# Optimization experiments

Measured on AMD Instinct MI355X. Metric: run time of the kernel, lower is better.

Reference implementation:

```python
import jax, jax.numpy as jnp
import numpy as np

N, E, L = 10000, 160000, 4
IN, HID, HEADS, OUT = 15, 128, 4, 5
C = HID              # per-head out_channels of TransformerConv
HC = HEADS * C       # concatenated width = 512
EPS = 1e-5


def _w(k, shape, fan_in):
    return (jax.random.normal(k, shape, jnp.float32) / np.sqrt(fan_in)).astype(jnp.float32)


def setup_inputs() -> dict:
    key = jax.random.key(0)
    ks = jax.random.split(key, 24)
    return {
        "x": jax.random.normal(ks[0], (N, IN), jnp.float32),
        "edge_index": jax.random.randint(ks[1], (2, E), 0, N, dtype=jnp.int32),
        # input / output projections
        "W_in": _w(ks[2], (IN, HID), IN), "b_in": jnp.zeros((HID,), jnp.float32),
        "W_out": _w(ks[3], (HID, OUT), HID), "b_out": jnp.zeros((OUT,), jnp.float32),
        # stacked per-layer TransformerConv params (L leading dim)
        "Wq": _w(ks[4], (L, HID, HC), HID), "bq": jnp.zeros((L, HC), jnp.float32),
        "Wk": _w(ks[5], (L, HID, HC), HID), "bk": jnp.zeros((L, HC), jnp.float32),
        "Wv": _w(ks[6], (L, HID, HC), HID), "bv": jnp.zeros((L, HC), jnp.float32),
        "Wskip": _w(ks[7], (L, HID, HC), HID), "bskip": jnp.zeros((L, HC), jnp.float32),
        "Wbeta": _w(ks[8], (L, 3 * HC, 1), 3 * HC),
        "ln_w": jnp.ones((L, HC), jnp.float32), "ln_b": jnp.zeros((L, HC), jnp.float32),
        "Wproj": _w(ks[9], (L, HC, HID), HC), "bproj": jnp.zeros((L, HID), jnp.float32),
    }


def _forward(x, edge_index, W_in, b_in, Wq, bq, Wk, bk, Wv, bv,
             Wskip, bskip, Wbeta, ln_w, ln_b, Wproj, bproj, W_out, b_out):
    src, dst = edge_index[0], edge_index[1]  # message j->i aggregated at dst
    h = x @ W_in + b_in  # [N, HID]

    def layer(h, p):
        Wq_, bq_, Wk_, bk_, Wv_, bv_, Ws_, bs_, Wb_, lw, lb, Wp_, bp_ = p
        q = (h @ Wq_ + bq_).reshape(N, HEADS, C)
        k = (h @ Wk_ + bk_).reshape(N, HEADS, C)
        v = (h @ Wv_ + bv_).reshape(N, HEADS, C)
        # attention logits per edge/head: [E, HEADS]
        logits = (q[dst] * k[src]).sum(-1) / jnp.sqrt(jnp.float32(C))
        # segment softmax over incoming edges of each target node
        m = jax.ops.segment_max(logits, dst, num_segments=N)
        ex = jnp.exp(logits - m[dst])
        den = jax.ops.segment_sum(ex, dst, num_segments=N)
        alpha = ex / (den[dst] + 1e-16)
        out = jax.ops.segment_sum(v[src] * alpha[..., None], dst,
                                  num_segments=N).reshape(N, HC)
        # beta-gated skip (TransformerConv beta=True)
        skip = h @ Ws_ + bs_
        beta = jax.nn.sigmoid(jnp.concatenate([out, skip, out - skip], -1) @ Wb_)  # [N,1]
        out = beta * skip + (1.0 - beta) * out
        # PyG LayerNorm, mode='graph' (single graph): normalize over all elements
        xc = out - out.mean()
        out = xc / (jnp.sqrt((xc * xc).mean()) + EPS) * lw + lb
        out = out @ Wp_ + bp_
        return jax.nn.relu(out + h), None

    params = (Wq, bq, Wk, bk, Wv, bv, Wskip, bskip, Wbeta, ln_w, ln_b, Wproj, bproj)
    h, _ = jax.lax.scan(layer, h, params)
    return h @ W_out + b_out


def reference(x, edge_index, W_in, b_in, Wq, bq, Wk, bk, Wv, bv,
              Wskip, bskip, Wbeta, ln_w, ln_b, Wproj, bproj, W_out, b_out):
    return _forward(x, edge_index, W_in, b_in, Wq, bq, Wk, bk, Wv, bv,
                    Wskip, bskip, Wbeta, ln_w, ln_b, Wproj, bproj, W_out, b_out)
```

## Files before the change

kernel.cpp:

```cpp
#include <hip/hip_runtime.h>
#include <math.h>

#define NN 10000
#define NE 160000
#define HCW 512
#define CH 128
#define NLAYERS 4
#define LN_EPS 1e-5f
#define NBUCK 128

typedef short bf16x8 __attribute__((ext_vector_type(8)));
typedef float f32x4 __attribute__((ext_vector_type(4)));

__device__ inline unsigned short f2bf(float f) {
    union { float f; unsigned int u; } x; x.f = f;
    unsigned int u = x.u;
    return (unsigned short)((u + 0x7FFFu + ((u >> 16) & 1u)) >> 16);
}
__device__ inline float bf2f(unsigned short s) {
    union { unsigned int u; float f; } x; x.u = ((unsigned int)s) << 16;
    return x.f;
}
__device__ inline float lo16(unsigned int u) {
    union { unsigned int x; float f; } v; v.x = u << 16; return v.f;
}
__device__ inline float hi16(unsigned int u) {
    union { unsigned int x; float f; } v; v.x = u & 0xffff0000u; return v.f;
}

template<int CTRL>
__device__ inline float dppadd(float x) {
    int y = __builtin_amdgcn_update_dpp(0, __float_as_int(x), CTRL, 0xF, 0xF, true);
    return x + __int_as_float(y);
}
__device__ inline float red16(float x) {
    x = dppadd<0x128>(x);
    x = dppadd<0x124>(x);
    x = dppadd<0x122>(x);
    x = dppadd<0x121>(x);
    return x;
}
__device__ inline float red64(float x) {
    x = red16(x);
    x += __shfl_xor(x, 16, 64);
    x += __shfl_xor(x, 32, 64);
    return x;
}

__device__ inline float dot8(const float4& q0, const float4& q1, const uint4& kk) {
    return q0.x * lo16(kk.x) + q0.y * hi16(kk.x)
         + q0.z * lo16(kk.y) + q0.w * hi16(kk.y)
         + q1.x * lo16(kk.z) + q1.y * hi16(kk.z)
         + q1.z * lo16(kk.w) + q1.w * hi16(kk.w);
}

__global__ void k_init(int* cnt, int* fill, float* stats) {
    int i = blockIdx.x * blockDim.x + threadIdx.x;
    if (i < NN) { cnt[i] = 0; fill[i] = 0; }
    if (i < NLAYERS * NBUCK * 16) stats[i] = 0.f;
}

__global__ void k_count(const int* __restrict__ dst, int* __restrict__ cnt) {
    int e = blockIdx.x * blockDim.x + threadIdx.x;
    if (e < NE) atomicAdd(&cnt[dst[e]], 1);
}

__global__ __launch_bounds__(1024) void k_scan(const int* __restrict__ cnt, int* __restrict__ offs) {
    __shared__ int sh[1024];
    __shared__ int carry;
    if (threadIdx.x == 0) carry = 0;
    __syncthreads();
    for (int base = 0; base < NN; base += 1024) {
        int i = base + threadIdx.x;
        int v = (i < NN) ? cnt[i] : 0;
        sh[threadIdx.x] = v;
        __syncthreads();
        for (int off = 1; off < 1024; off <<= 1) {
            int t = (threadIdx.x >= off) ? sh[threadIdx.x - off] : 0;
            __syncthreads();
            sh[threadIdx.x] += t;
            __syncthreads();
        }
        int incl = sh[threadIdx.x];
        if (i < NN) offs[i] = carry + incl - v;
        __syncthreads();
        if (threadIdx.x == 1023) carry += sh[1023];
        __syncthreads();
    }
    if (threadIdx.x == 0) offs[NN] = carry;
}

__global__ void k_fill(const int* __restrict__ src, const int* __restrict__ dst,
                       const int* __restrict__ offs, int* __restrict__ fill,
                       int* __restrict__ col) {
    int e = blockIdx.x * blockDim.x + threadIdx.x;
    if (e < NE) {
        int d = dst[e];
        int p = offs[d] + atomicAdd(&fill[d], 1);
        col[p] = src[e];
    }
}

__global__ void k_wconv(const float* __restrict__ Wq, const float* __restrict__ Wk,
                        const float* __restrict__ Wv, const float* __restrict__ Ws,
                        const float* __restrict__ Wp,
                        unsigned short* __restrict__ wt_qkvs,
                        unsigned short* __restrict__ wpt) {
    int id = blockIdx.x * blockDim.x + threadIdx.x;
    if (id < NLAYERS * 2048 * 128) {
        int l = id >> 18;
        int rem = id & 262143;
        int n = rem >> 7, k = rem & 127;
        int mat = n >> 9, wcol = n & 511;
        const float* W = (mat == 0) ? Wq : (mat == 1) ? Wk : (mat == 2) ? Wv : Ws;
        wt_qkvs[id] = f2bf(W[(size_t)l * 65536 + k * 512 + wcol]);
    } else if (id < NLAYERS * 2048 * 128 + NLAYERS * 128 * 512) {
        int id2 = id - NLAYERS * 2048 * 128;
        int l = id2 >> 16;
        int rem = id2 & 65535;
        int n = rem >> 9, k = rem & 511;
        wpt[(size_t)l * 65536 + n * 512 + k] = f2bf(Wp[(size_t)l * 65536 + k * 128 + n]);
    }
}

__global__ __launch_bounds__(128) void k_inproj(const float* __restrict__ x,
                                                const float* __restrict__ W,
                                                const float* __restrict__ b,
                                                float* __restrict__ h,
                                                unsigned short* __restrict__ h_bf) {
    int n = blockIdx.x;
    int j = threadIdx.x;
    float acc = b[j];
#pragma unroll
    for (int i = 0; i < 15; i++) acc += x[n * 15 + i] * W[i * 128 + j];
    h[n * 128 + j] = acc;
    h_bf[n * 128 + j] = f2bf(acc);
}

__global__ __launch_bounds__(256) void k_qkvs_mfma(
    const unsigned short* __restrict__ h_bf,
    const unsigned short* __restrict__ Wt,
    const float* __restrict__ bq, const float* __restrict__ bk,
    const float* __restrict__ bv, const float* __restrict__ bs,
    unsigned short* __restrict__ qb16, unsigned short* __restrict__ kv16,
    unsigned short* __restrict__ sb16) {
    __shared__ unsigned short As[128 * 128];
    __shared__ unsigned short Bs[128 * 128];
    int row0 = blockIdx.x * 128;
    int n0 = blockIdx.y * 128;
    int t = threadIdx.x;
#pragma unroll
    for (int i = 0; i < 8; i++) {
        int c = t + i * 256;
        int r = c >> 4, cc = c & 15;
        int gr = row0 + r;
        uint4 v = make_uint4(0, 0, 0, 0);
        if (gr < NN) v = *(const uint4*)(h_bf + (size_t)gr * 128 + cc * 8);
        int sc = (r << 4) | (cc ^ (r & 7));
        *(uint4*)(As + sc * 8) = v;
    }
#pragma unroll
    for (int i = 0; i < 8; i++) {
        int c = t + i * 256;
        int r = c >> 4, cc = c & 15;
        uint4 v = *(const uint4*)(Wt + (size_t)(n0 + r) * 128 + cc * 8);
        int sc = (r << 4) | (cc ^ (r & 7));
        *(uint4*)(Bs + sc * 8) = v;
    }
    __syncthreads();
    int wave = t >> 6, lane = t & 63;
    int wr = (wave >> 1) * 64, wc = (wave & 1) * 64;
    int lr = lane & 15, lk = lane >> 4;
    f32x4 acc[4][4] = {};
#pragma unroll
    for (int ks = 0; ks < 4; ks++) {
        bf16x8 a[4], b[4];
#pragma unroll
        for (int mi = 0; mi < 4; mi++) {
            int r = wr + mi * 16 + lr;
            int cc = (ks * 4 + lk) ^ (r & 7);
            a[mi] = *(const bf16x8*)(As + (((r << 4) | cc) * 8));
        }
#pragma unroll
        for (int ni = 0; ni < 4; ni++) {
            int r = wc + ni * 16 + lr;
            int cc = (ks * 4 + lk) ^ (r & 7);
            b[ni] = *(const bf16x8*)(Bs + (((r << 4) | cc) * 8));
        }
#pragma unroll
        for (int mi = 0; mi < 4; mi++)
#pragma unroll
            for (int ni = 0; ni < 4; ni++)
                acc[mi][ni] = __builtin_amdgcn_mfma_f32_16x16x32_bf16(a[mi], b[ni], acc[mi][ni], 0, 0, 0);
    }
    int mat = blockIdx.y >> 2;
    int wcol0 = n0 & 511;
    const float* bias_p = (mat == 0) ? bq : (mat == 1) ? bk : (mat == 2) ? bv : bs;
    __syncthreads();
#pragma unroll
    for (int ni = 0; ni < 4; ni++) {
        int colL = wc + ni * 16 + lr;
        float bias = bias_p[wcol0 + colL];
#pragma unroll
        for (int mi = 0; mi < 4; mi++) {
            int rowB = wr + mi * 16 + 4 * lk;
#pragma unroll
            for (int r = 0; r < 4; r++) {
                int row = rowB + r;
                unsigned int w = (unsigned int)(row * 64 + (colL >> 1));
                w ^= ((row >> 2) & 7) << 3;
                As[w * 2 + (colL & 1)] = f2bf(acc[mi][ni][r] + bias);
            }
        }
    }
    __syncthreads();
    unsigned short* outp = (mat == 0) ? qb16 : (mat == 3) ? sb16 : kv16;
    int rowStride = (mat == 1 || mat == 2) ? 1024 : 512;
    int cbase = wcol0 + ((mat == 2) ? 512 : 0);
#pragma unroll
    for (int i = 0; i < 8; i++) {
        int idx = t + i * 256;
        int row2 = idx >> 4;
        int c8 = (idx & 15) * 8;
        int gr = row0 + row2;
        if (gr < NN) {
            unsigned int wb = (unsigned int)(row2 * 64 + (idx & 15) * 4);
            wb ^= ((row2 >> 2) & 7) << 3;
            uint4 v = *(const uint4*)(As + wb * 2);
            *(uint4*)(outp + (size_t)gr * rowStride + cbase + c8) = v;
        }
    }
}

__global__ __launch_bounds__(256) void k_attn_beta(
    const unsigned short* __restrict__ qb16,
    const unsigned short* __restrict__ kv16,
    const unsigned short* __restrict__ sb16,
    const float* __restrict__ Wb,
    const int* __restrict__ offs, const int* __restrict__ col,
    unsigned short* __restrict__ gated16, float* __restrict__ stats) {
    int n = blockIdx.x;
    int head = threadIdx.x >> 6;
    int lane = threadIdx.x & 63;
    int g = lane >> 4;
    int subl = lane & 15;
    const int hbase = head * CH;
    const int off = hbase + subl * 8;
    uint4 qq = *(const uint4*)(qb16 + (size_t)n * HCW + off);
    float4 q0 = {lo16(qq.x), hi16(qq.x), lo16(qq.y), hi16(qq.y)};
    float4 q1 = {lo16(qq.z), hi16(qq.z), lo16(qq.w), hi16(qq.w)};
    int beg = offs[n], end = offs[n + 1];
    const float scale = 0.08838834764831845f;

    float mA = -INFINITY, sA = 0.f, mB = -INFINITY, sB = 0.f;
    float4 a0A = {0.f, 0.f, 0.f, 0.f}, a1A = {0.f, 0.f, 0.f, 0.f};
    float4 a0B = {0.f, 0.f, 0.f, 0.f}, a1B = {0.f, 0.f, 0.f, 0.f};

    for (int p = beg + g; p < end; p += 8) {
        int pB = p + 4;
        bool hasB = (pB < end);
        int snA = col[p];
        int snB = hasB ? col[pB] : snA;
        const unsigned short* bA = kv16 + ((size_t)snA << 10) + off;
        const unsigned short* bB = kv16 + ((size_t)snB << 10) + off;
        uint4 kkA = *(const uint4*)bA;
        uint4 vvA = *(const uint4*)(bA + 512);
        uint4 kkB = *(const uint4*)bB;
        uint4 vvB = *(const uint4*)(bB + 512);
        float dA = dot8(q0, q1, kkA);
        float dB = dot8(q0, q1, kkB);
        dA = red16(dA);
        dB = red16(dB);
        float lA = dA * scale;
        float lB = dB * scale;
        if (lA <= mA + 8.f) {
            float w = __expf(lA - mA);
            sA += w;
            a0A.x += w * lo16(vvA.x); a0A.y += w * hi16(vvA.x);
            a0A.z += w * lo16(vvA.y); a0A.w += w * hi16(vvA.y);
            a1A.x += w * lo16(vvA.z); a1A.y += w * hi16(vvA.z);
            a1A.z += w * lo16(vvA.w); a1A.w += w * hi16(vvA.w);
        } else {
            float sc = __expf(mA - lA);
            sA = sA * sc + 1.f;
            a0A.x = a0A.x * sc + lo16(vvA.x); a0A.y = a0A.y * sc + hi16(vvA.x);
            a0A.z = a0A.z * sc + lo16(vvA.y); a0A.w = a0A.w * sc + hi16(vvA.y);
            a1A.x = a1A.x * sc + lo16(vvA.z); a1A.y = a1A.y * sc + hi16(vvA.z);
            a1A.z = a1A.z * sc + lo16(vvA.w); a1A.w = a1A.w * sc + hi16(vvA.w);
            mA = lA;
        }
        if (hasB) {
            if (lB <= mB + 8.f) {
                float w = __expf(lB - mB);
                sB += w;
                a0B.x += w * lo16(vvB.x); a0B.y += w * hi16(vvB.x);
                a0B.z += w * lo16(vvB.y); a0B.w += w * hi16(vvB.y);
                a1B.x += w * lo16(vvB.z); a1B.y += w * hi16(vvB.z);
                a1B.z += w * lo16(vvB.w); a1B.w += w * hi16(vvB.w);
            } else {
                float sc = __expf(mB - lB);
                sB = sB * sc + 1.f;
                a0B.x = a0B.x * sc + lo16(vvB.x); a0B.y = a0B.y * sc + hi16(vvB.x);
                a0B.z = a0B.z * sc + lo16(vvB.y); a0B.w = a0B.w * sc + hi16(vvB.y);
                a1B.x = a1B.x * sc + lo16(vvB.z); a1B.y = a1B.y * sc + hi16(vvB.z);
                a1B.z = a1B.z * sc + lo16(vvB.w); a1B.w = a1B.w * sc + hi16(vvB.w);
                mB = lB;
            }
        }
    }
    {
        float mn = fmaxf(mA, mB);
        float c1 = (sA > 0.f) ? __expf(mA - mn) : 0.f;
        float c2 = (sB > 0.f) ? __expf(mB - mn) : 0.f;
        sA = sA * c1 + sB * c2;
        a0A.x = a0A.x * c1 + a0B.x * c2; a0A.y = a0A.y * c1 + a0B.y * c2;
        a0A.z = a0A.z * c1 + a0B.z * c2; a0A.w = a0A.w * c1 + a0B.w * c2;
        a1A.x = a1A.x * c1 + a1B.x * c2; a1A.y = a1A.y * c1 + a1B.y * c2;
        a1A.z = a1A.z * c1 + a1B.z * c2; a1A.w = a1A.w * c1 + a1B.w * c2;
        mA = mn;
    }
#pragma unroll
    for (int off2 = 16; off2 <= 32; off2 <<= 1) {
        float m_o = __shfl_xor(mA, off2, 64);
        float s_o = __shfl_xor(sA, off2, 64);
        float4 b0, b1;
        b0.x = __shfl_xor(a0A.x, off2, 64); b0.y = __shfl_xor(a0A.y, off2, 64);
        b0.z = __shfl_xor(a0A.z, off2, 64); b0.w = __shfl_xor(a0A.w, off2, 64);
        b1.x = __shfl_xor(a1A.x, off2, 64); b1.y = __shfl_xor(a1A.y, off2, 64);
        b1.z = __shfl_xor(a1A.z, off2, 64); b1.w = __shfl_xor(a1A.w, off2, 64);
        float mn = fmaxf(mA, m_o);
        float c1 = (sA > 0.f) ? __expf(mA - mn) : 0.f;
        float c2 = (s_o > 0.f) ? __expf(m_o - mn) : 0.f;
        sA = sA * c1 + s_o * c2;
        a0A.x = a0A.x * c1 + b0.x * c2; a0A.y = a0A.y * c1 + b0.y * c2;
        a0A.z = a0A.z * c1 + b0.z * c2; a0A.w = a0A.w * c1 + b0.w * c2;
        a1A.x = a1A.x * c1 + b1.x * c2; a1A.y = a1A.y * c1 + b1.y * c2;
        a1A.z = a1A.z * c1 + b1.z * c2; a1A.w = a1A.w * c1 + b1.w * c2;
        mA = mn;
    }
    float inv = (sA > 0.f) ? 1.f / sA : 0.f;

    __shared__ float att_s[512];
    if (g == 0) {
        float4 o0 = {a0A.x * inv, a0A.y * inv, a0A.z * inv, a0A.w * inv};
        float4 o1 = {a1A.x * inv, a1A.y * inv, a1A.z * inv, a1A.w * inv};
        *(float4*)(att_s + off) = o0;
        *(float4*)(att_s + off + 4) = o1;
    }
    __syncthreads();

    int c0 = hbase + lane * 2;
    float o0 = att_s[c0], o1 = att_s[c0 + 1];
    unsigned int sku = *(const unsigned int*)(sb16 + (size_t)n * HCW + c0);
    float skx = lo16(sku), sky = hi16(sku);
    float part = o0 * Wb[c0] + o1 * Wb[c0 + 1]
               + skx * Wb[512 + c0] + sky * Wb[512 + c0 + 1]
               + (o0 - skx) * Wb[1024 + c0] + (o1 - sky) * Wb[1024 + c0 + 1];
    part = red64(part);
    __shared__ float red[4];
    if (lane == 0) red[head] = part;
    __syncthreads();
    float tot = red[0] + red[1] + red[2] + red[3];
    float beta = 1.f / (1.f + __expf(-tot));
    float gx = beta * skx + (1.f - beta) * o0;
    float gy = beta * sky + (1.f - beta) * o1;
    unsigned int gu = (unsigned int)f2bf(gx) | ((unsigned int)f2bf(gy) << 16);
    *(unsigned int*)(gated16 + (size_t)n * HCW + c0) = gu;

    float gxr = lo16(gu), gyr = hi16(gu);
    float ls = red64(gxr + gyr);
    float lq = red64(gxr * gxr + gyr * gyr);
    __shared__ float r2[8];
    if (lane == 0) { r2[head] = ls; r2[4 + head] = lq; }
    __syncthreads();
    if (threadIdx.x == 0) {
        int b = n & (NBUCK - 1);
        atomicAdd(&stats[b * 16], r2[0] + r2[1] + r2[2] + r2[3]);
        atomicAdd(&stats[b * 16 + 1], r2[4] + r2[5] + r2[6] + r2[7]);
    }
}

__global__ __launch_bounds__(512) void k_proj_mfma(
    const unsigned short* __restrict__ gated16,
    const unsigned short* __restrict__ Wpt,
    const float* __restrict__ bp,
    const float* __restrict__ lw, const float* __restrict__ lb,
    const float* __restrict__ stats,
    float* __restrict__ h, unsigned short* __restrict__ h_bf) {
    __shared__ unsigned short As[64 * 128];
    __shared__ unsigned short Bs[128 * 128];
    int row0 = blockIdx.x * 64;
    int t = threadIdx.x;
    float ssum = 0.f, sq = 0.f;
#pragma unroll 16
    for (int i = 0; i < NBUCK; i++) { ssum += stats[i * 16]; sq += stats[i * 16 + 1]; }
    const float invM = 1.f / (NN * 512.f);
    float mean = ssum * invM;
    float ms = sq * invM - mean * mean;
    float rstd = 1.f / (sqrtf(fmaxf(ms, 0.f)) + LN_EPS);
    int wave = t >> 6, lane = t & 63;
    int wr = (wave >> 1) * 16, wc = (wave & 1) * 64;
    int lr = lane & 15, lk = lane >> 4;
    f32x4 acc[4] = {};
    for (int kc = 0; kc < 4; kc++) {
        __syncthreads();
#pragma unroll
        for (int i = 0; i < 2; i++) {
            int c = t + i * 512;
            int r = c >> 4, cc = c & 15;
            int gr = row0 + r;
            int gk = kc * 128 + cc * 8;
            unsigned short u[8];
            if (gr < NN) {
                uint4 gv = *(const uint4*)(gated16 + (size_t)gr * 512 + gk);
                float vals[8] = {lo16(gv.x), hi16(gv.x), lo16(gv.y), hi16(gv.y),
                                 lo16(gv.z), hi16(gv.z), lo16(gv.w), hi16(gv.w)};
#pragma unroll
                for (int j = 0; j < 8; j++)
                    u[j] = f2bf((vals[j] - mean) * rstd * lw[gk + j] + lb[gk + j]);
            } else {
#pragma unroll
                for (int j = 0; j < 8; j++) u[j] = 0;
            }
            int sc = (r << 4) | (cc ^ (r & 7));
            *(uint4*)(As + sc * 8) = *(uint4*)u;
        }
#pragma unroll
        for (int i = 0; i < 4; i++) {
            int c = t + i * 512;
            int r = c >> 4, cc = c & 15;
            uint4 v = *(const uint4*)(Wpt + (size_t)r * 512 + kc * 128 + cc * 8);
            int sc = (r << 4) | (cc ^ (r & 7));
            *(uint4*)(Bs + sc * 8) = v;
        }
        __syncthreads();
#pragma unroll
        for (int ks = 0; ks < 4; ks++) {
            bf16x8 a, b[4];
            {
                int r = wr + lr;
                int cc = (ks * 4 + lk) ^ (r & 7);
                a = *(const bf16x8*)(As + (((r << 4) | cc) * 8));
            }
#pragma unroll
            for (int ni = 0; ni < 4; ni++) {
                int r = wc + ni * 16 + lr;
                int cc = (ks * 4 + lk) ^ (r & 7);
                b[ni] = *(const bf16x8*)(Bs + (((r << 4) | cc) * 8));
            }
#pragma unroll
            for (int ni = 0; ni < 4; ni++)
                acc[ni] = __builtin_amdgcn_mfma_f32_16x16x32_bf16(a, b[ni], acc[ni], 0, 0, 0);
        }
    }
#pragma unroll
    for (int ni = 0; ni < 4; ni++) {
        int gc = wc + ni * 16 + lr;
        float bias = bp[gc];
        int gr0 = row0 + wr + 4 * lk;
#pragma unroll
        for (int r = 0; r < 4; r++) {
            int grr = gr0 + r;
            if (grr < NN) {
                float o = acc[ni][r] + bias + h[(size_t)grr * 128 + gc];
                o = fmaxf(o, 0.f);
                h[(size_t)grr * 128 + gc] = o;
                h_bf[(size_t)grr * 128 + gc] = f2bf(o);
            }
        }
    }
}

__global__ void k_out(const float* __restrict__ h, const float* __restrict__ W,
                      const float* __restrict__ b, float* __restrict__ out) {
    int i = blockIdx.x * blockDim.x + threadIdx.x;
    if (i >= NN * 5) return;
    int n = i / 5, j = i % 5;
    float acc = b[j];
    for (int k = 0; k < 128; k++) acc += h[(size_t)n * 128 + k] * W[k * 5 + j];
    out[i] = acc;
}

extern "C" void kernel_launch(void* const* d_in, const int* in_sizes, int n_in,
                              void* d_out, int out_size, void* d_ws, size_t ws_size,
                              hipStream_t stream) {
    const float* x     = (const float*)d_in[0];
    const int* ei      = (const int*)d_in[1];
    const float* W_in  = (const float*)d_in[2];
    const float* b_in  = (const float*)d_in[3];
    const float* W_out = (const float*)d_in[4];
    const float* b_out = (const float*)d_in[5];
    const float* Wq    = (const float*)d_in[6];
    const float* bq    = (const float*)d_in[7];
    const float* Wk    = (const float*)d_in[8];
    const float* bk    = (const float*)d_in[9];
    const float* Wv    = (const float*)d_in[10];
    const float* bv    = (const float*)d_in[11];
    const float* Wsk   = (const float*)d_in[12];
    const float* bsk   = (const float*)d_in[13];
    const float* Wbeta = (const float*)d_in[14];
    const float* ln_w  = (const float*)d_in[15];
    const float* ln_b  = (const float*)d_in[16];
    const float* Wproj = (const float*)d_in[17];
    const float* bproj = (const float*)d_in[18];
    float* out = (float*)d_out;

    float* h     = (float*)d_ws;
    float* stats = h + (size_t)NN * 128;
    int* offs = (int*)(stats + NLAYERS * NBUCK * 16);
    int* cnt  = offs + (NN + 1);
    int* fill = cnt + NN;
    int* col  = fill + NN;
    unsigned short* h_bf = (unsigned short*)(((uintptr_t)(col + NE) + 15) & ~(uintptr_t)15);
    unsigned short* qb16 = h_bf + (size_t)NN * 128;
    unsigned short* sb16 = qb16 + (size_t)NN * 512;
    unsigned short* kv16 = sb16 + (size_t)NN * 512;
    unsigned short* wt_qkvs = kv16 + (size_t)NN * 1024;
    unsigned short* wpt = wt_qkvs + (size_t)NLAYERS * 2048 * 128;
    unsigned short* gated16 = qb16;

    const int* src = ei;
    const int* dst = ei + NE;

    k_init<<<(NN + 255) / 256, 256, 0, stream>>>(cnt, fill, stats);
    k_count<<<(NE + 255) / 256, 256, 0, stream>>>(dst, cnt);
    k_scan<<<1, 1024, 0, stream>>>(cnt, offs);
    k_fill<<<(NE + 255) / 256, 256, 0, stream>>>(src, dst, offs, fill, col);
    {
        int tot = NLAYERS * 2048 * 128 + NLAYERS * 128 * 512;
        k_wconv<<<(tot + 255) / 256, 256, 0, stream>>>(Wq, Wk, Wv, Wsk, Wproj, wt_qkvs, wpt);
    }
    k_inproj<<<NN, 128, 0, stream>>>(x, W_in, b_in, h, h_bf);

    for (int l = 0; l < NLAYERS; ++l) {
        const unsigned short* Wt_ = wt_qkvs + (size_t)l * 2048 * 128;
        const unsigned short* Wp_ = wpt + (size_t)l * 128 * 512;
        const float* bq_ = bq + l * 512;
        const float* bk_ = bk + l * 512;
        const float* bv_ = bv + l * 512;
        const float* bs_ = bsk + l * 512;
        const float* Wb_ = Wbeta + (size_t)l * 1536;
        const float* lw_ = ln_w + l * 512;
        const float* lb_ = ln_b + l * 512;
        const float* bp_ = bproj + l * 128;
        float* st = stats + (size_t)l * NBUCK * 16;

        dim3 g1((NN + 127) / 128, 16);
        k_qkvs_mfma<<<g1, 256, 0, stream>>>(h_bf, Wt_, bq_, bk_, bv_, bs_,
                                            qb16, kv16, sb16);
        k_attn_beta<<<NN, 256, 0, stream>>>(qb16, kv16, sb16, Wb_, offs, col, gated16, st);
        k_proj_mfma<<<(NN + 63) / 64, 512, 0, stream>>>(gated16, Wp_, bp_, lw_, lb_, st, h, h_bf);
    }
    k_out<<<(NN * 5 + 255) / 256, 256, 0, stream>>>(h, W_out, b_out, out);
}
```

Measured before the change: 453.0 us.

## Map one wavefront per node in attention kernel with 4-edge unrolled gathers

The attention/beta kernel now assigns one 64-lane wavefront per destination node (4 nodes per block) instead of a whole 256-thread block per node. Each lane covers 8 channels across all heads, and the edge loop gathers 4 neighbors at once into independent online-softmax accumulators. This removes the cross-wave LDS exchange, two __syncthreads, and the cross-group shuffle merge, and raises memory-level parallelism per lane. The trade-off is more registers per thread, and each edge's gather now goes through a single wave serially rather than across 4 edge groups, so per-node latency for high-degree nodes grows.

```diff
diff --git a/kernel.cpp b/kernel.cpp
--- a/kernel.cpp
+++ b/kernel.cpp
@@ -239,142 +239,108 @@
     const float* __restrict__ Wb,
     const int* __restrict__ offs, const int* __restrict__ col,
     unsigned short* __restrict__ gated16, float* __restrict__ stats) {
-    int n = blockIdx.x;
-    int head = threadIdx.x >> 6;
+    int wave = threadIdx.x >> 6;
     int lane = threadIdx.x & 63;
-    int g = lane >> 4;
-    int subl = lane & 15;
-    const int hbase = head * CH;
-    const int off = hbase + subl * 8;
+    int n = blockIdx.x * 4 + wave;
+    const int off = ((lane >> 4) << 7) + ((lane & 15) << 3);
     uint4 qq = *(const uint4*)(qb16 + (size_t)n * HCW + off);
     float4 q0 = {lo16(qq.x), hi16(qq.x), lo16(qq.y), hi16(qq.y)};
     float4 q1 = {lo16(qq.z), hi16(qq.z), lo16(qq.w), hi16(qq.w)};
     int beg = offs[n], end = offs[n + 1];
     const float scale = 0.08838834764831845f;
 
-    float mA = -INFINITY, sA = 0.f, mB = -INFINITY, sB = 0.f;
-    float4 a0A = {0.f, 0.f, 0.f, 0.f}, a1A = {0.f, 0.f, 0.f, 0.f};
-    float4 a0B = {0.f, 0.f, 0.f, 0.f}, a1B = {0.f, 0.f, 0.f, 0.f};
-
-    for (int p = beg + g; p < end; p += 8) {
-        int pB = p + 4;
-        bool hasB = (pB < end);
-        int snA = col[p];
-        int snB = hasB ? col[pB] : snA;
-        const unsigned short* bA = kv16 + ((size_t)snA << 10) + off;
-        const unsigned short* bB = kv16 + ((size_t)snB << 10) + off;
-        uint4 kkA = *(const uint4*)bA;
-        uint4 vvA = *(const uint4*)(bA + 512);
-        uint4 kkB = *(const uint4*)bB;
-        uint4 vvB = *(const uint4*)(bB + 512);
-        float dA = dot8(q0, q1, kkA);
-        float dB = dot8(q0, q1, kkB);
-        dA = red16(dA);
-        dB = red16(dB);
-        float lA = dA * scale;
-        float lB = dB * scale;
-        if (lA <= mA + 8.f) {
-            float w = __expf(lA - mA);
-            sA += w;
-            a0A.x += w * lo16(vvA.x); a0A.y += w * hi16(vvA.x);
-            a0A.z += w * lo16(vvA.y); a0A.w += w * hi16(vvA.y);
-            a1A.x += w * lo16(vvA.z); a1A.y += w * hi16(vvA.z);
-            a1A.z += w * lo16(vvA.w); a1A.w += w * hi16(vvA.w);
-        } else {
-            float sc = __expf(mA - lA);
-            sA = sA * sc + 1.f;
-            a0A.x = a0A.x * sc + lo16(vvA.x); a0A.y = a0A.y * sc + hi16(vvA.x);
-            a0A.z = a0A.z * sc + lo16(vvA.y); a0A.w = a0A.w * sc + hi16(vvA.y);
-            a1A.x = a1A.x * sc + lo16(vvA.z); a1A.y = a1A.y * sc + hi16(vvA.z);
-            a1A.z = a1A.z * sc + lo16(vvA.w); a1A.w = a1A.w * sc + hi16(vvA.w);
-            mA = lA;
-        }
-        if (hasB) {
-            if (lB <= mB + 8.f) {
-                float w = __expf(lB - mB);
-                sB += w;
-                a0B.x += w * lo16(vvB.x); a0B.y += w * hi16(vvB.x);
-                a0B.z += w * lo16(vvB.y); a0B.w += w * hi16(vvB.y);
-                a1B.x += w * lo16(vvB.z); a1B.y += w * hi16(vvB.z);
-                a1B.z += w * lo16(vvB.w); a1B.w += w * hi16(vvB.w);
+    float m[4], s[4];
+    float4 a0[4], a1[4];
+#pragma unroll
+    for (int i = 0; i < 4; i++) {
+        m[i] = -INFINITY; s[i] = 0.f;
+        a0[i] = make_float4(0.f, 0.f, 0.f, 0.f);
+        a1[i] = make_float4(0.f, 0.f, 0.f, 0.f);
+    }
+
+    for (int p = beg; p < end; p += 4) {
+        uint4 kk[4], vv[4];
+        bool has[4];
+#pragma unroll
+        for (int i = 0; i < 4; i++) {
+            int pi = p + i;
+            has[i] = (pi < end);
+            int sn = col[has[i] ? pi : p];
+            const unsigned short* bp_ = kv16 + ((size_t)sn << 10) + off;
+            kk[i] = *(const uint4*)bp_;
+            vv[i] = *(const uint4*)(bp_ + 512);
+        }
+#pragma unroll
+        for (int i = 0; i < 4; i++) {
+            if (!has[i]) continue;
+            float l = red16(dot8(q0, q1, kk[i])) * scale;
+            if (l <= m[i] + 8.f) {
+                float w = __expf(l - m[i]);
+                s[i] += w;
+                a0[i].x += w * lo16(vv[i].x); a0[i].y += w * hi16(vv[i].x);
+                a0[i].z += w * lo16(vv[i].y); a0[i].w += w * hi16(vv[i].y);
+                a1[i].x += w * lo16(vv[i].z); a1[i].y += w * hi16(vv[i].z);
+                a1[i].z += w * lo16(vv[i].w); a1[i].w += w * hi16(vv[i].w);
             } else {
-                float sc = __expf(mB - lB);
-                sB = sB * sc + 1.f;
-                a0B.x = a0B.x * sc + lo16(vvB.x); a0B.y = a0B.y * sc + hi16(vvB.x);
-                a0B.z = a0B.z * sc + lo16(vvB.y); a0B.w = a0B.w * sc + hi16(vvB.y);
-                a1B.x = a1B.x * sc + lo16(vvB.z); a1B.y = a1B.y * sc + hi16(vvB.z);
-                a1B.z = a1B.z * sc + lo16(vvB.w); a1B.w = a1B.w * sc + hi16(vvB.w);
-                mB = lB;
+                float sc = __expf(m[i] - l);
+                s[i] = s[i] * sc + 1.f;
+                a0[i].x = a0[i].x * sc + lo16(vv[i].x); a0[i].y = a0[i].y * sc + hi16(vv[i].x);
+                a0[i].z = a0[i].z * sc + lo16(vv[i].y); a0[i].w = a0[i].w * sc + hi16(vv[i].y);
+                a1[i].x = a1[i].x * sc + lo16(vv[i].z); a1[i].y = a1[i].y * sc + hi16(vv[i].z);
+                a1[i].z = a1[i].z * sc + lo16(vv[i].w); a1[i].w = a1[i].w * sc + hi16(vv[i].w);
+                m[i] = l;
             }
         }
     }
-    {
-        float mn = fmaxf(mA, mB);
-        float c1 = (sA > 0.f) ? __expf(mA - mn) : 0.f;
-        float c2 = (sB > 0.f) ? __expf(mB - mn) : 0.f;
-        sA = sA * c1 + sB * c2;
-        a0A.x = a0A.x * c1 + a0B.x * c2; a0A.y = a0A.y * c1 + a0B.y * c2;
-        a0A.z = a0A.z * c1 + a0B.z * c2; a0A.w = a0A.w * c1 + a0B.w * c2;
-        a1A.x = a1A.x * c1 + a1B.x * c2; a1A.y = a1A.y * c1 + a1B.y * c2;
-        a1A.z = a1A.z * c1 + a1B.z * c2; a1A.w = a1A.w * c1 + a1B.w * c2;
-        mA = mn;
-    }
-#pragma unroll
-    for (int off2 = 16; off2 <= 32; off2 <<= 1) {
-        float m_o = __shfl_xor(mA, off2, 64);
-        float s_o = __shfl_xor(sA, off2, 64);
-        float4 b0, b1;
-        b0.x = __shfl_xor(a0A.x, off2, 64); b0.y = __shfl_xor(a0A.y, off2, 64);
-        b0.z = __shfl_xor(a0A.z, off2, 64); b0.w = __shfl_xor(a0A.w, off2, 64);
-        b1.x = __shfl_xor(a1A.x, off2, 64); b1.y = __shfl_xor(a1A.y, off2, 64);
-        b1.z = __shfl_xor(a1A.z, off2, 64); b1.w = __shfl_xor(a1A.w, off2, 64);
-        float mn = fmaxf(mA, m_o);
-        float c1 = (sA > 0.f) ? __expf(mA - mn) : 0.f;
-        float c2 = (s_o > 0.f) ? __expf(m_o - mn) : 0.f;
-        sA = sA * c1 + s_o * c2;
-        a0A.x = a0A.x * c1 + b0.x * c2; a0A.y = a0A.y * c1 + b0.y * c2;
-        a0A.z = a0A.z * c1 + b0.z * c2; a0A.w = a0A.w * c1 + b0.w * c2;
-        a1A.x = a1A.x * c1 + b1.x * c2; a1A.y = a1A.y * c1 + b1.y * c2;
-        a1A.z = a1A.z * c1 + b1.z * c2; a1A.w = a1A.w * c1 + b1.w * c2;
-        mA = mn;
-    }
-    float inv = (sA > 0.f) ? 1.f / sA : 0.f;
-
-    __shared__ float att_s[512];
-    if (g == 0) {
-        float4 o0 = {a0A.x * inv, a0A.y * inv, a0A.z * inv, a0A.w * inv};
-        float4 o1 = {a1A.x * inv, a1A.y * inv, a1A.z * inv, a1A.w * inv};
-        *(float4*)(att_s + off) = o0;
-        *(float4*)(att_s + off + 4) = o1;
-    }
-    __syncthreads();
-
-    int c0 = hbase + lane * 2;
-    float o0 = att_s[c0], o1 = att_s[c0 + 1];
-    unsigned int sku = *(const unsigned int*)(sb16 + (size_t)n * HCW + c0);
-    float skx = lo16(sku), sky = hi16(sku);
-    float part = o0 * Wb[c0] + o1 * Wb[c0 + 1]
-               + skx * Wb[512 + c0] + sky * Wb[512 + c0 + 1]
-               + (o0 - skx) * Wb[1024 + c0] + (o1 - sky) * Wb[1024 + c0 + 1];
+#pragma unroll
+    for (int i = 1; i < 4; i++) {
+        float mn = fmaxf(m[0], m[i]);
+        float c1 = (s[0] > 0.f) ? __expf(m[0] - mn) : 0.f;
+        float c2 = (s[i] > 0.f) ? __expf(m[i] - mn) : 0.f;
+        s[0] = s[0] * c1 + s[i] * c2;
+        a0[0].x = a0[0].x * c1 + a0[i].x * c2; a0[0].y = a0[0].y * c1 + a0[i].y * c2;
+        a0[0].z = a0[0].z * c1 + a0[i].z * c2; a0[0].w = a0[0].w * c1 + a0[i].w * c2;
+        a1[0].x = a1[0].x * c1 + a1[i].x * c2; a1[0].y = a1[0].y * c1 + a1[i].y * c2;
+        a1[0].z = a1[0].z * c1 + a1[i].z * c2; a1[0].w = a1[0].w * c1 + a1[i].w * c2;
+        m[0] = mn;
+    }
+    float inv = (s[0] > 0.f) ? 1.f / s[0] : 0.f;
+    float o[8] = {a0[0].x * inv, a0[0].y * inv, a0[0].z * inv, a0[0].w * inv,
+                  a1[0].x * inv, a1[0].y * inv, a1[0].z * inv, a1[0].w * inv};
+
+    uint4 sku = *(const uint4*)(sb16 + (size_t)n * HCW + off);
+    float sk[8] = {lo16(sku.x), hi16(sku.x), lo16(sku.y), hi16(sku.y),
+                   lo16(sku.z), hi16(sku.z), lo16(sku.w), hi16(sku.w)};
+
+    float part = 0.f;
+#pragma unroll
+    for (int j = 0; j < 8; j++) {
+        int c = off + j;
+        part += o[j] * Wb[c] + sk[j] * Wb[512 + c] + (o[j] - sk[j]) * Wb[1024 + c];
+    }
     part = red64(part);
-    __shared__ float red[4];
-    if (lane == 0) red[head] = part;
-    __syncthreads();
-    float tot = red[0] + red[1] + red[2] + red[3];
-    float beta = 1.f / (1.f + __expf(-tot));
-    float gx = beta * skx + (1.f - beta) * o0;
-    float gy = beta * sky + (1.f - beta) * o1;
-    unsigned int gu = (unsigned int)f2bf(gx) | ((unsigned int)f2bf(gy) << 16);
-    *(unsigned int*)(gated16 + (size_t)n * HCW + c0) = gu;
-
-    float gxr = lo16(gu), gyr = hi16(gu);
-    float ls = red64(gxr + gyr);
-    float lq = red64(gxr * gxr + gyr * gyr);
+    float beta = 1.f / (1.f + __expf(-part));
+
+    unsigned int gu[4];
+    float ls = 0.f, lq = 0.f;
+#pragma unroll
+    for (int j = 0; j < 4; j++) {
+        float gx = beta * sk[2 * j] + (1.f - beta) * o[2 * j];
+        float gy = beta * sk[2 * j + 1] + (1.f - beta) * o[2 * j + 1];
+        gu[j] = (unsigned int)f2bf(gx) | ((unsigned int)f2bf(gy) << 16);
+        float gxr = lo16(gu[j]), gyr = hi16(gu[j]);
+        ls += gxr + gyr;
+        lq += gxr * gxr + gyr * gyr;
+    }
+    *(uint4*)(gated16 + (size_t)n * HCW + off) = *(uint4*)gu;
+
+    ls = red64(ls);
+    lq = red64(lq);
     __shared__ float r2[8];
-    if (lane == 0) { r2[head] = ls; r2[4 + head] = lq; }
+    if (lane == 0) { r2[wave] = ls; r2[4 + wave] = lq; }
     __syncthreads();
     if (threadIdx.x == 0) {
-        int b = n & (NBUCK - 1);
+        int b = blockIdx.x & (NBUCK - 1);
         atomicAdd(&stats[b * 16], r2[0] + r2[1] + r2[2] + r2[3]);
         atomicAdd(&stats[b * 16 + 1], r2[4] + r2[5] + r2[6] + r2[7]);
     }
@@ -548,7 +514,7 @@
         dim3 g1((NN + 127) / 128, 16);
         k_qkvs_mfma<<<g1, 256, 0, stream>>>(h_bf, Wt_, bq_, bk_, bv_, bs_,
                                             qb16, kv16, sb16);
-        k_attn_beta<<<NN, 256, 0, stream>>>(qb16, kv16, sb16, Wb_, offs, col, gated16, st);
+        k_attn_beta<<<NN / 4, 256, 0, stream>>>(qb16, kv16, sb16, Wb_, offs, col, gated16, st);
         k_proj_mfma<<<(NN + 63) / 64, 512, 0, stream>>>(gated16, Wp_, bp_, lw_, lb_, st, h, h_bf);
     }
     k_out<<<(NN * 5 + 255) / 256, 256, 0, stream>>>(h, W_out, b_out, out);
```

Result: no change. 448.8 us (-0.9%).
